# Optimization experiments

Hardware: AMD Instinct MI355X
Metric: run time of the kernel (lower is better)

## Reference

```python
import jax, jax.numpy as jnp
import numpy as np

B, D = 256, 1024
EPS = 1e-6


def setup_inputs() -> dict:
    key = jax.random.key(0)
    ks = jax.random.split(key, 8)
    s = 1.0 / np.sqrt(D)
    return {
        "x": jax.random.normal(ks[0], (B, D), jnp.float32),
        "Wq": jax.random.normal(ks[1], (D, D), jnp.float32) * s,
        "bq": jax.random.normal(ks[2], (D,), jnp.float32) * 0.01,
        "Wk": jax.random.normal(ks[3], (D, D), jnp.float32) * s,
        "bk": jax.random.normal(ks[4], (D,), jnp.float32) * 0.01,
        "Wv": jax.random.normal(ks[5], (D, D), jnp.float32) * s,
        "bv": jax.random.normal(ks[6], (D,), jnp.float32) * 0.01,
        "scale": jnp.asarray(1.0, jnp.float32),
        "norm_w": jnp.ones((D,), jnp.float32),
    }


def reference(x, Wq, bq, Wk, bk, Wv, bv, scale, norm_w):
    # QKV projections (torch Linear: x @ W.T + b)
    Q = x @ Wq.T + bq  # [B, D]
    K = x @ Wk.T + bk  # [B, D]
    V = x @ Wv.T + bv  # [B, D]
    # outer-product scores [B, D, D]: scores[b,i,j] = Q[b,i]*K[b,j]/scale
    scores = (Q[:, :, None] * K[:, None, :]) / scale
    attn = jax.nn.softmax(scores, axis=-1)  # [B, D, D]
    attended = jnp.einsum("bij,bj->bi", attn, V)  # [B, D]
    # dropout is identity in eval mode
    h = attended + x
    rms = jnp.sqrt(jnp.mean(h * h, axis=-1, keepdims=True) + EPS)
    return (h / rms) * norm_w
```

## Files before the change

### kernel.cpp

```cpp
#include <hip/hip_runtime.h>
#include <hip/hip_bf16.h>

#define BB 256
#define DD 1024

typedef unsigned short u16;
typedef unsigned int   u32;
typedef __attribute__((ext_vector_type(8))) __bf16 bf16x8;
typedef __attribute__((ext_vector_type(4))) float  floatx4;

__device__ __forceinline__ float bf2f(u16 u) {
    union { u32 i; float f; } t; t.i = ((u32)u) << 16; return t.f;
}
__device__ __forceinline__ u16 f2bf_rne(float f) {
    u32 u = __float_as_uint(f);
    u32 r = u + 0x7FFFu + ((u >> 16) & 1u);
    return (u16)(r >> 16);
}
__device__ __forceinline__ bool detect_bf16(const void* p) {
    return (*(const u32*)p) == 0x3F803F80u;
}
__device__ __forceinline__ float loadf(const void* p, int i, bool bf) {
    return bf ? bf2f(((const u16*)p)[i]) : ((const float*)p)[i];
}

__device__ __forceinline__ float wave_sum64(float x) {
    x += __int_as_float(__builtin_amdgcn_update_dpp(0, __float_as_int(x), 0x111, 0xF, 0xF, true));
    x += __int_as_float(__builtin_amdgcn_update_dpp(0, __float_as_int(x), 0x112, 0xF, 0xF, true));
    x += __int_as_float(__builtin_amdgcn_update_dpp(0, __float_as_int(x), 0x114, 0xF, 0xF, true));
    x += __int_as_float(__builtin_amdgcn_update_dpp(0, __float_as_int(x), 0x118, 0xF, 0xF, true));
    x += __int_as_float(__builtin_amdgcn_update_dpp(0, __float_as_int(x), 0x142, 0xA, 0xF, true));
    x += __int_as_float(__builtin_amdgcn_update_dpp(0, __float_as_int(x), 0x143, 0xC, 0xF, true));
    return x;
}

__device__ __forceinline__ void split1(float f, u16& h, u16& l) {
    u32 u  = __float_as_uint(f);
    u32 hu = u & 0xFFFF0000u;
    h = (u16)(hu >> 16);
    l = f2bf_rne(f - __uint_as_float(hu));
}

__global__ __launch_bounds__(256) void qkv_gemm(
    const void* __restrict__ x,
    const void* __restrict__ Wq, const void* __restrict__ bq,
    const void* __restrict__ Wk, const void* __restrict__ bk,
    const void* __restrict__ Wv, const void* __restrict__ bv,
    const void* __restrict__ nw,
    float* __restrict__ qkv)
{
    const bool bf = detect_bf16(nw);
    const int z = blockIdx.z;
    const void* W    = (z == 0) ? Wq : (z == 1) ? Wk : Wv;
    const void* bias = (z == 0) ? bq : (z == 1) ? bk : bv;
    float* outp = qkv + (size_t)z * BB * DD;

    const int m0 = blockIdx.x * 32;
    const int n0 = blockIdx.y * 64;
    const int tid  = threadIdx.x;
    const int lane = tid & 63;
    const int wave = tid >> 6;
    const int wr = wave & 1, wc = wave >> 1;
    const int l15 = lane & 15, quad = lane >> 4;

    __shared__ __align__(16) u16 Ah[32][72], Al[32][72];
    __shared__ __align__(16) u16 Bh[64][72], Bl[64][72];

    const int arow = tid >> 4;
    const int acol = (tid & 15) * 4;

    floatx4 acc[2] = {(floatx4){0.f,0.f,0.f,0.f}, (floatx4){0.f,0.f,0.f,0.f}};

    float4 ar[2], br[4];
    auto ld4 = [&](const void* p, int idx) -> float4 {
        if (!bf) return *(const float4*)((const float*)p + idx);
        const u16* q = (const u16*)p + idx;
        return make_float4(bf2f(q[0]), bf2f(q[1]), bf2f(q[2]), bf2f(q[3]));
    };
    auto fetch = [&](int k0) {
        #pragma unroll
        for (int f = 0; f < 2; ++f) ar[f] = ld4(x, (m0 + arow + f * 16) * DD + k0 + acol);
        #pragma unroll
        for (int f = 0; f < 4; ++f) br[f] = ld4(W, (n0 + arow + f * 16) * DD + k0 + acol);
    };

    fetch(0);
    for (int k0 = 0; k0 < DD; k0 += 64) {
        #pragma unroll
        for (int f = 0; f < 2; ++f) {
            const int r = arow + f * 16;
            ushort4 h, l;
            split1(ar[f].x, h.x, l.x); split1(ar[f].y, h.y, l.y);
            split1(ar[f].z, h.z, l.z); split1(ar[f].w, h.w, l.w);
            *(ushort4*)&Ah[r][acol] = h;
            *(ushort4*)&Al[r][acol] = l;
        }
        #pragma unroll
        for (int f = 0; f < 4; ++f) {
            const int r = arow + f * 16;
            ushort4 h, l;
            split1(br[f].x, h.x, l.x); split1(br[f].y, h.y, l.y);
            split1(br[f].z, h.z, l.z); split1(br[f].w, h.w, l.w);
            *(ushort4*)&Bh[r][acol] = h;
            *(ushort4*)&Bl[r][acol] = l;
        }
        __syncthreads();

        fetch((k0 + 64) & (DD - 1));

        #pragma unroll
        for (int kk = 0; kk < 2; ++kk) {
            const int ko = kk * 32 + quad * 8;
            const bf16x8 ah = *(const bf16x8*)&Ah[wr * 16 + l15][ko];
            const bf16x8 al = *(const bf16x8*)&Al[wr * 16 + l15][ko];
            #pragma unroll
            for (int ni = 0; ni < 2; ++ni) {
                const int brow = wc * 32 + ni * 16 + l15;
                const bf16x8 bh = *(const bf16x8*)&Bh[brow][ko];
                const bf16x8 bl = *(const bf16x8*)&Bl[brow][ko];
                acc[ni] = __builtin_amdgcn_mfma_f32_16x16x32_bf16(al, bh, acc[ni], 0, 0, 0);
                acc[ni] = __builtin_amdgcn_mfma_f32_16x16x32_bf16(ah, bl, acc[ni], 0, 0, 0);
                acc[ni] = __builtin_amdgcn_mfma_f32_16x16x32_bf16(ah, bh, acc[ni], 0, 0, 0);
            }
        }
        __syncthreads();
    }

    #pragma unroll
    for (int ni = 0; ni < 2; ++ni) {
        const int ng = n0 + wc * 32 + ni * 16 + l15;
        const float bv_ = loadf(bias, ng, bf);
        #pragma unroll
        for (int reg = 0; reg < 4; ++reg) {
            const int mg = m0 + wr * 16 + quad * 4 + reg;
            outp[mg * DD + ng] = acc[ni][reg] + bv_;
        }
    }
}

__global__ __launch_bounds__(1024) void attn_norm(
    const float* __restrict__ qkv,
    const void* __restrict__ x,
    const void* __restrict__ scale_p,
    const void* __restrict__ norm_w,
    void* __restrict__ out)
{
    const bool bf = detect_bf16(norm_w);
    const int b = blockIdx.x;
    const int tid = threadIdx.x;
    const int lane = tid & 63;
    const int wave = tid >> 6;

    __shared__ __align__(16) float2 kv[DD];
    __shared__ float wsum[16];

    const float* Qp = qkv + (size_t)b * DD;
    const float* Kp = Qp + (size_t)BB * DD;
    const float* Vp = Qp + 2 * (size_t)BB * DD;
    const float cvt = 1.44269504088896f / loadf(scale_p, 0, bf);

    kv[tid] = make_float2(Kp[tid] * cvt, Vp[tid]);
    __syncthreads();

    const float q   = Qp[tid];
    const float x_l = loadf(x, b * DD + tid, bf);

    float S0 = 0.f, S1 = 0.f, S2 = 0.f, S3 = 0.f;
    float T0 = 0.f, T1 = 0.f, T2 = 0.f, T3 = 0.f;
    const float4* kv4 = (const float4*)kv;
    for (int m = 0; m < DD / 2; m += 4) {
        const float4 p0 = kv4[m + 0];
        const float4 p1 = kv4[m + 1];
        const float4 p2 = kv4[m + 2];
        const float4 p3 = kv4[m + 3];
        float e;
        e = __builtin_amdgcn_exp2f(q * p0.x); S0 += e; T0 = fmaf(e, p0.y, T0);
        e = __builtin_amdgcn_exp2f(q * p0.z); S1 += e; T1 = fmaf(e, p0.w, T1);
        e = __builtin_amdgcn_exp2f(q * p1.x); S2 += e; T2 = fmaf(e, p1.y, T2);
        e = __builtin_amdgcn_exp2f(q * p1.z); S3 += e; T3 = fmaf(e, p1.w, T3);
        e = __builtin_amdgcn_exp2f(q * p2.x); S0 += e; T0 = fmaf(e, p2.y, T0);
        e = __builtin_amdgcn_exp2f(q * p2.z); S1 += e; T1 = fmaf(e, p2.w, T1);
        e = __builtin_amdgcn_exp2f(q * p3.x); S2 += e; T2 = fmaf(e, p3.y, T2);
        e = __builtin_amdgcn_exp2f(q * p3.z); S3 += e; T3 = fmaf(e, p3.w, T3);
    }
    const float S = (S0 + S1) + (S2 + S3);
    const float T = (T0 + T1) + (T2 + T3);
    const float h = fmaf(T, __builtin_amdgcn_rcpf(S), x_l);

    const float ss = wave_sum64(h * h);
    if (lane == 63) wsum[wave] = ss;
    __syncthreads();
    float tot = 0.f;
    #pragma unroll
    for (int w = 0; w < 16; ++w) tot += wsum[w];
    const float rinv = __builtin_amdgcn_rsqf(tot * (1.0f / DD) + 1e-6f);
    const float val = h * rinv * loadf(norm_w, tid, bf);
    const size_t oi = (size_t)b * DD + tid;
    if (bf) ((u16*)out)[oi] = f2bf_rne(val);
    else    ((float*)out)[oi] = val;
}

extern "C" void kernel_launch(void* const* d_in, const int* in_sizes, int n_in,
                              void* d_out, int out_size, void* d_ws, size_t ws_size,
                              hipStream_t stream) {
    const void* x  = d_in[0];
    const void* Wq = d_in[1];
    const void* bq = d_in[2];
    const void* Wk = d_in[3];
    const void* bk = d_in[4];
    const void* Wv = d_in[5];
    const void* bv = d_in[6];
    const void* sc = d_in[7];
    const void* nw = d_in[8];

    float* qkv = (float*)d_ws;

    qkv_gemm<<<dim3(8, 16, 3), 256, 0, stream>>>(x, Wq, bq, Wk, bk, Wv, bv, nw, qkv);
    attn_norm<<<dim3(BB), 1024, 0, stream>>>(qkv, x, sc, nw, d_out);
}
```

Before: 132.6 us.

## Pre-split inputs to bf16 hi/lo and run split-term GEMMs with atomic accumulation

Adds a prepass kernel that converts x and the three weight matrices into bf16 high/low halves in workspace and seeds the QKV output with biases. A new LDS-free GEMM reads the pre-split operands straight from global memory into registers with double-buffered fetches, and runs each of the three split products (lo*hi, hi*lo, hi*hi) as separate grid slices that atomically add into the output. The attention kernel drops its shared K/V staging and reads K/V directly from global memory with 8 accumulators. This trades redundant per-tile splitting and LDS traffic for an extra pass over the weights, more launches, and float atomics that make summation order nondeterministic.

```diff
diff --git a/kernel.cpp b/kernel.cpp
--- a/kernel.cpp
+++ b/kernel.cpp
@@ -22,6 +22,22 @@
 }
 __device__ __forceinline__ float loadf(const void* p, int i, bool bf) {
     return bf ? bf2f(((const u16*)p)[i]) : ((const float*)p)[i];
+}
+__device__ __forceinline__ float4 ld4(const void* p, int idx, bool bf) {
+    if (!bf) return *(const float4*)((const float*)p + idx);
+    const u16* q = (const u16*)p + idx;
+    return make_float4(bf2f(q[0]), bf2f(q[1]), bf2f(q[2]), bf2f(q[3]));
+}
+
+__device__ __forceinline__ void split1(float f, u16& h, u16& l) {
+    u32 u  = __float_as_uint(f);
+    u32 hu = u & 0xFFFF0000u;
+    h = (u16)(hu >> 16);
+    l = f2bf_rne(f - __uint_as_float(hu));
+}
+__device__ __forceinline__ void split4(float4 f, ushort4& h, ushort4& l) {
+    split1(f.x, h.x, l.x); split1(f.y, h.y, l.y);
+    split1(f.z, h.z, l.z); split1(f.w, h.w, l.w);
 }
 
 __device__ __forceinline__ float wave_sum64(float x) {
@@ -34,11 +50,108 @@
     return x;
 }
 
-__device__ __forceinline__ void split1(float f, u16& h, u16& l) {
-    u32 u  = __float_as_uint(f);
-    u32 hu = u & 0xFFFF0000u;
-    h = (u16)(hu >> 16);
-    l = f2bf_rne(f - __uint_as_float(hu));
+__global__ __launch_bounds__(256) void prepass(
+    const void* __restrict__ x,
+    const void* __restrict__ Wq, const void* __restrict__ Wk, const void* __restrict__ Wv,
+    const void* __restrict__ bq, const void* __restrict__ bk, const void* __restrict__ bv,
+    const void* __restrict__ nw,
+    float* __restrict__ qkv, u16* __restrict__ Xh, u16* __restrict__ Xl,
+    u16* __restrict__ Wh, u16* __restrict__ Wl)
+{
+    const bool bf = detect_bf16(nw);
+    const int idx = blockIdx.x * 256 + threadIdx.x;
+    if (idx < 65536) {
+        const int e = idx * 4;
+        ushort4 h, l; split4(ld4(x, e, bf), h, l);
+        *(ushort4*)(Xh + e) = h;
+        *(ushort4*)(Xl + e) = l;
+    } else if (idx < 65536 + 786432) {
+        const int i2 = idx - 65536;
+        const int wz = i2 >> 18;
+        const int e  = (i2 & 262143) * 4;
+        const void* W = (wz == 0) ? Wq : (wz == 1) ? Wk : Wv;
+        ushort4 h, l; split4(ld4(W, e, bf), h, l);
+        *(ushort4*)(Wh + wz * 1048576 + e) = h;
+        *(ushort4*)(Wl + wz * 1048576 + e) = l;
+    } else {
+        const int i3 = idx - (65536 + 786432);
+        const int z  = i3 >> 16;
+        const int e  = (i3 & 65535) * 4;
+        const void* B = (z == 0) ? bq : (z == 1) ? bk : bv;
+        *(float4*)(qkv + z * 262144 + e) = ld4(B, e & 1023, bf);
+    }
+}
+
+__global__ __launch_bounds__(256) void gemm_split(
+    const u16* __restrict__ Xh, const u16* __restrict__ Xl,
+    const u16* __restrict__ Wh, const u16* __restrict__ Wl,
+    float* __restrict__ qkv)
+{
+    const int seg = blockIdx.z / 3;
+    const int z   = blockIdx.z % 3;
+    const u16* Ap = (seg == 1) ? Xl : Xh;
+    const u16* Bp = ((seg == 2) ? Wl : Wh) + z * 1048576;
+    float* C = qkv + z * 262144;
+
+    const int m0 = blockIdx.x * 64, n0 = blockIdx.y * 64;
+    const int lane = threadIdx.x & 63;
+    const int wave = threadIdx.x >> 6;
+    const int wr = wave & 1, wc = wave >> 1;
+    const int l15 = lane & 15, quad = lane >> 4;
+
+    const u16* aRow[2]; const u16* bRow[2];
+    #pragma unroll
+    for (int mi = 0; mi < 2; ++mi) aRow[mi] = Ap + (m0 + wr * 32 + mi * 16 + l15) * DD + quad * 8;
+    #pragma unroll
+    for (int ni = 0; ni < 2; ++ni) bRow[ni] = Bp + (n0 + wc * 32 + ni * 16 + l15) * DD + quad * 8;
+
+    floatx4 acc[2][2];
+    #pragma unroll
+    for (int mi = 0; mi < 2; ++mi)
+        #pragma unroll
+        for (int ni = 0; ni < 2; ++ni)
+            acc[mi][ni] = (floatx4){0.f, 0.f, 0.f, 0.f};
+
+    bf16x8 fa0[2][2], fb0[2][2], fa1[2][2], fb1[2][2];
+    auto fetch = [&](bf16x8 (&fa)[2][2], bf16x8 (&fb)[2][2], int k0) {
+        #pragma unroll
+        for (int kk = 0; kk < 2; ++kk) {
+            #pragma unroll
+            for (int mi = 0; mi < 2; ++mi) fa[kk][mi] = *(const bf16x8*)(aRow[mi] + k0 + kk * 32);
+            #pragma unroll
+            for (int ni = 0; ni < 2; ++ni) fb[kk][ni] = *(const bf16x8*)(bRow[ni] + k0 + kk * 32);
+        }
+    };
+    auto compute = [&](bf16x8 (&fa)[2][2], bf16x8 (&fb)[2][2]) {
+        #pragma unroll
+        for (int kk = 0; kk < 2; ++kk)
+            #pragma unroll
+            for (int mi = 0; mi < 2; ++mi)
+                #pragma unroll
+                for (int ni = 0; ni < 2; ++ni)
+                    acc[mi][ni] = __builtin_amdgcn_mfma_f32_16x16x32_bf16(
+                        fa[kk][mi], fb[kk][ni], acc[mi][ni], 0, 0, 0);
+    };
+
+    fetch(fa0, fb0, 0);
+    for (int k0 = 0; k0 < DD; k0 += 128) {
+        fetch(fa1, fb1, k0 + 64);
+        compute(fa0, fb0);
+        if (k0 + 128 < DD) fetch(fa0, fb0, k0 + 128);
+        compute(fa1, fb1);
+    }
+
+    #pragma unroll
+    for (int ni = 0; ni < 2; ++ni) {
+        const int ng = n0 + wc * 32 + ni * 16 + l15;
+        #pragma unroll
+        for (int mi = 0; mi < 2; ++mi)
+            #pragma unroll
+            for (int reg = 0; reg < 4; ++reg) {
+                const int mg = m0 + wr * 32 + mi * 16 + quad * 4 + reg;
+                atomicAdd(&C[mg * DD + ng], acc[mi][ni][reg]);
+            }
+    }
 }
 
 __global__ __launch_bounds__(256) void qkv_gemm(
@@ -72,42 +185,29 @@
     floatx4 acc[2] = {(floatx4){0.f,0.f,0.f,0.f}, (floatx4){0.f,0.f,0.f,0.f}};
 
     float4 ar[2], br[4];
-    auto ld4 = [&](const void* p, int idx) -> float4 {
-        if (!bf) return *(const float4*)((const float*)p + idx);
-        const u16* q = (const u16*)p + idx;
-        return make_float4(bf2f(q[0]), bf2f(q[1]), bf2f(q[2]), bf2f(q[3]));
-    };
     auto fetch = [&](int k0) {
         #pragma unroll
-        for (int f = 0; f < 2; ++f) ar[f] = ld4(x, (m0 + arow + f * 16) * DD + k0 + acol);
-        #pragma unroll
-        for (int f = 0; f < 4; ++f) br[f] = ld4(W, (n0 + arow + f * 16) * DD + k0 + acol);
+        for (int f = 0; f < 2; ++f) ar[f] = ld4(x, (m0 + arow + f * 16) * DD + k0 + acol, bf);
+        #pragma unroll
+        for (int f = 0; f < 4; ++f) br[f] = ld4(W, (n0 + arow + f * 16) * DD + k0 + acol, bf);
     };
 
     fetch(0);
     for (int k0 = 0; k0 < DD; k0 += 64) {
         #pragma unroll
         for (int f = 0; f < 2; ++f) {
-            const int r = arow + f * 16;
-            ushort4 h, l;
-            split1(ar[f].x, h.x, l.x); split1(ar[f].y, h.y, l.y);
-            split1(ar[f].z, h.z, l.z); split1(ar[f].w, h.w, l.w);
-            *(ushort4*)&Ah[r][acol] = h;
-            *(ushort4*)&Al[r][acol] = l;
+            ushort4 h, l; split4(ar[f], h, l);
+            *(ushort4*)&Ah[arow + f * 16][acol] = h;
+            *(ushort4*)&Al[arow + f * 16][acol] = l;
         }
         #pragma unroll
         for (int f = 0; f < 4; ++f) {
-            const int r = arow + f * 16;
-            ushort4 h, l;
-            split1(br[f].x, h.x, l.x); split1(br[f].y, h.y, l.y);
-            split1(br[f].z, h.z, l.z); split1(br[f].w, h.w, l.w);
-            *(ushort4*)&Bh[r][acol] = h;
-            *(ushort4*)&Bl[r][acol] = l;
+            ushort4 h, l; split4(br[f], h, l);
+            *(ushort4*)&Bh[arow + f * 16][acol] = h;
+            *(ushort4*)&Bl[arow + f * 16][acol] = l;
         }
         __syncthreads();
-
         fetch((k0 + 64) & (DD - 1));
-
         #pragma unroll
         for (int kk = 0; kk < 2; ++kk) {
             const int ko = kk * 32 + quad * 8;
@@ -125,7 +225,6 @@
         }
         __syncthreads();
     }
-
     #pragma unroll
     for (int ni = 0; ni < 2; ++ni) {
         const int ng = n0 + wc * 32 + ni * 16 + l15;
@@ -151,42 +250,32 @@
     const int lane = tid & 63;
     const int wave = tid >> 6;
 
-    __shared__ __align__(16) float2 kv[DD];
-    __shared__ float wsum[16];
-
     const float* Qp = qkv + (size_t)b * DD;
     const float* Kp = Qp + (size_t)BB * DD;
     const float* Vp = Qp + 2 * (size_t)BB * DD;
+
     const float cvt = 1.44269504088896f / loadf(scale_p, 0, bf);
-
-    kv[tid] = make_float2(Kp[tid] * cvt, Vp[tid]);
-    __syncthreads();
-
-    const float q   = Qp[tid];
+    const float qc  = Qp[tid] * cvt;
     const float x_l = loadf(x, b * DD + tid, bf);
 
-    float S0 = 0.f, S1 = 0.f, S2 = 0.f, S3 = 0.f;
-    float T0 = 0.f, T1 = 0.f, T2 = 0.f, T3 = 0.f;
-    const float4* kv4 = (const float4*)kv;
-    for (int m = 0; m < DD / 2; m += 4) {
-        const float4 p0 = kv4[m + 0];
-        const float4 p1 = kv4[m + 1];
-        const float4 p2 = kv4[m + 2];
-        const float4 p3 = kv4[m + 3];
-        float e;
-        e = __builtin_amdgcn_exp2f(q * p0.x); S0 += e; T0 = fmaf(e, p0.y, T0);
-        e = __builtin_amdgcn_exp2f(q * p0.z); S1 += e; T1 = fmaf(e, p0.w, T1);
-        e = __builtin_amdgcn_exp2f(q * p1.x); S2 += e; T2 = fmaf(e, p1.y, T2);
-        e = __builtin_amdgcn_exp2f(q * p1.z); S3 += e; T3 = fmaf(e, p1.w, T3);
-        e = __builtin_amdgcn_exp2f(q * p2.x); S0 += e; T0 = fmaf(e, p2.y, T0);
-        e = __builtin_amdgcn_exp2f(q * p2.z); S1 += e; T1 = fmaf(e, p2.w, T1);
-        e = __builtin_amdgcn_exp2f(q * p3.x); S2 += e; T2 = fmaf(e, p3.y, T2);
-        e = __builtin_amdgcn_exp2f(q * p3.z); S3 += e; T3 = fmaf(e, p3.w, T3);
-    }
-    const float S = (S0 + S1) + (S2 + S3);
-    const float T = (T0 + T1) + (T2 + T3);
-    const float h = fmaf(T, __builtin_amdgcn_rcpf(S), x_l);
-
+    float S[8], T[8];
+    #pragma unroll
+    for (int u = 0; u < 8; ++u) { S[u] = 0.f; T[u] = 0.f; }
+
+    #pragma unroll 2
+    for (int j = 0; j < DD; j += 8) {
+        #pragma unroll
+        for (int u = 0; u < 8; ++u) {
+            const float e = __builtin_amdgcn_exp2f(qc * Kp[j + u]);
+            S[u] += e;
+            T[u] = fmaf(e, Vp[j + u], T[u]);
+        }
+    }
+    const float Ssum = ((S[0] + S[1]) + (S[2] + S[3])) + ((S[4] + S[5]) + (S[6] + S[7]));
+    const float Tsum = ((T[0] + T[1]) + (T[2] + T[3])) + ((T[4] + T[5]) + (T[6] + T[7]));
+    const float h = fmaf(Tsum, __builtin_amdgcn_rcpf(Ssum), x_l);
+
+    __shared__ float wsum[16];
     const float ss = wave_sum64(h * h);
     if (lane == 63) wsum[wave] = ss;
     __syncthreads();
@@ -215,6 +304,16 @@
 
     float* qkv = (float*)d_ws;
 
-    qkv_gemm<<<dim3(8, 16, 3), 256, 0, stream>>>(x, Wq, bq, Wk, bk, Wv, bv, nw, qkv);
+    if (ws_size >= (size_t)16 * 1024 * 1024) {
+        u16* Xh = (u16*)(qkv + 786432);
+        u16* Xl = Xh + 262144;
+        u16* Wh = Xl + 262144;
+        u16* Wl = Wh + 3 * 1048576;
+        prepass<<<dim3(4096), 256, 0, stream>>>(x, Wq, Wk, Wv, bq, bk, bv, nw,
+                                                qkv, Xh, Xl, Wh, Wl);
+        gemm_split<<<dim3(4, 16, 9), 256, 0, stream>>>(Xh, Xl, Wh, Wl, qkv);
+    } else {
+        qkv_gemm<<<dim3(8, 16, 3), 256, 0, stream>>>(x, Wq, bq, Wk, bk, Wv, bv, nw, qkv);
+    }
     attn_norm<<<dim3(BB), 1024, 0, stream>>>(qkv, x, sc, nw, d_out);
 }
```

Measured after the change: 161.0 us. 21.4% more time.

## Split attention into finer blocks, separate RMSNorm kernel, skip low split for bf16

Applied to the files above, without the earlier changes.

The 1024-thread-per-batch attention+norm kernel becomes a 256-thread kernel launched four times per batch row. Each block recomputes the K/V staging and writes the residual sum in place over Q, and a new finalize kernel does the RMS normalisation with vectorised loads and stores. The goal is better occupancy and more independent accumulators in the exp-heavy inner loop, paid for with an extra launch and a global round trip. The GEMM also drops the low-part bf16 split and its two extra MFMAs when inputs are bf16, but the default fp32 inputs do not take that path.

```diff
diff --git a/kernel.cpp b/kernel.cpp
--- a/kernel.cpp
+++ b/kernel.cpp
@@ -23,7 +23,21 @@
 __device__ __forceinline__ float loadf(const void* p, int i, bool bf) {
     return bf ? bf2f(((const u16*)p)[i]) : ((const float*)p)[i];
 }
-
+__device__ __forceinline__ float4 ld4(const void* p, int idx, bool bf) {
+    if (!bf) return *(const float4*)((const float*)p + idx);
+    const ushort4 q = *(const ushort4*)((const u16*)p + idx);
+    return make_float4(bf2f(q.x), bf2f(q.y), bf2f(q.z), bf2f(q.w));
+}
+__device__ __forceinline__ void split1(float f, u16& h, u16& l) {
+    u32 u  = __float_as_uint(f);
+    u32 hu = u & 0xFFFF0000u;
+    h = (u16)(hu >> 16);
+    l = f2bf_rne(f - __uint_as_float(hu));
+}
+__device__ __forceinline__ void split4(float4 f, ushort4& h, ushort4& l) {
+    split1(f.x, h.x, l.x); split1(f.y, h.y, l.y);
+    split1(f.z, h.z, l.z); split1(f.w, h.w, l.w);
+}
 __device__ __forceinline__ float wave_sum64(float x) {
     x += __int_as_float(__builtin_amdgcn_update_dpp(0, __float_as_int(x), 0x111, 0xF, 0xF, true));
     x += __int_as_float(__builtin_amdgcn_update_dpp(0, __float_as_int(x), 0x112, 0xF, 0xF, true));
@@ -32,13 +46,6 @@
     x += __int_as_float(__builtin_amdgcn_update_dpp(0, __float_as_int(x), 0x142, 0xA, 0xF, true));
     x += __int_as_float(__builtin_amdgcn_update_dpp(0, __float_as_int(x), 0x143, 0xC, 0xF, true));
     return x;
-}
-
-__device__ __forceinline__ void split1(float f, u16& h, u16& l) {
-    u32 u  = __float_as_uint(f);
-    u32 hu = u & 0xFFFF0000u;
-    h = (u16)(hu >> 16);
-    l = f2bf_rne(f - __uint_as_float(hu));
 }
 
 __global__ __launch_bounds__(256) void qkv_gemm(
@@ -57,9 +64,7 @@
 
     const int m0 = blockIdx.x * 32;
     const int n0 = blockIdx.y * 64;
-    const int tid  = threadIdx.x;
-    const int lane = tid & 63;
-    const int wave = tid >> 6;
+    const int tid = threadIdx.x, lane = tid & 63, wave = tid >> 6;
     const int wr = wave & 1, wc = wave >> 1;
     const int l15 = lane & 15, quad = lane >> 4;
 
@@ -72,54 +77,43 @@
     floatx4 acc[2] = {(floatx4){0.f,0.f,0.f,0.f}, (floatx4){0.f,0.f,0.f,0.f}};
 
     float4 ar[2], br[4];
-    auto ld4 = [&](const void* p, int idx) -> float4 {
-        if (!bf) return *(const float4*)((const float*)p + idx);
-        const u16* q = (const u16*)p + idx;
-        return make_float4(bf2f(q[0]), bf2f(q[1]), bf2f(q[2]), bf2f(q[3]));
-    };
     auto fetch = [&](int k0) {
         #pragma unroll
-        for (int f = 0; f < 2; ++f) ar[f] = ld4(x, (m0 + arow + f * 16) * DD + k0 + acol);
-        #pragma unroll
-        for (int f = 0; f < 4; ++f) br[f] = ld4(W, (n0 + arow + f * 16) * DD + k0 + acol);
+        for (int f = 0; f < 2; ++f) ar[f] = ld4(x, (m0 + arow + f * 16) * DD + k0 + acol, bf);
+        #pragma unroll
+        for (int f = 0; f < 4; ++f) br[f] = ld4(W, (n0 + arow + f * 16) * DD + k0 + acol, bf);
     };
 
     fetch(0);
     for (int k0 = 0; k0 < DD; k0 += 64) {
         #pragma unroll
         for (int f = 0; f < 2; ++f) {
-            const int r = arow + f * 16;
-            ushort4 h, l;
-            split1(ar[f].x, h.x, l.x); split1(ar[f].y, h.y, l.y);
-            split1(ar[f].z, h.z, l.z); split1(ar[f].w, h.w, l.w);
-            *(ushort4*)&Ah[r][acol] = h;
-            *(ushort4*)&Al[r][acol] = l;
+            ushort4 h, l; split4(ar[f], h, l);
+            *(ushort4*)&Ah[arow + f * 16][acol] = h;
+            if (!bf) *(ushort4*)&Al[arow + f * 16][acol] = l;
         }
         #pragma unroll
         for (int f = 0; f < 4; ++f) {
-            const int r = arow + f * 16;
-            ushort4 h, l;
-            split1(br[f].x, h.x, l.x); split1(br[f].y, h.y, l.y);
-            split1(br[f].z, h.z, l.z); split1(br[f].w, h.w, l.w);
-            *(ushort4*)&Bh[r][acol] = h;
-            *(ushort4*)&Bl[r][acol] = l;
+            ushort4 h, l; split4(br[f], h, l);
+            *(ushort4*)&Bh[arow + f * 16][acol] = h;
+            if (!bf) *(ushort4*)&Bl[arow + f * 16][acol] = l;
         }
         __syncthreads();
-
         fetch((k0 + 64) & (DD - 1));
-
         #pragma unroll
         for (int kk = 0; kk < 2; ++kk) {
             const int ko = kk * 32 + quad * 8;
             const bf16x8 ah = *(const bf16x8*)&Ah[wr * 16 + l15][ko];
-            const bf16x8 al = *(const bf16x8*)&Al[wr * 16 + l15][ko];
             #pragma unroll
             for (int ni = 0; ni < 2; ++ni) {
                 const int brow = wc * 32 + ni * 16 + l15;
                 const bf16x8 bh = *(const bf16x8*)&Bh[brow][ko];
-                const bf16x8 bl = *(const bf16x8*)&Bl[brow][ko];
-                acc[ni] = __builtin_amdgcn_mfma_f32_16x16x32_bf16(al, bh, acc[ni], 0, 0, 0);
-                acc[ni] = __builtin_amdgcn_mfma_f32_16x16x32_bf16(ah, bl, acc[ni], 0, 0, 0);
+                if (!bf) {
+                    const bf16x8 al = *(const bf16x8*)&Al[wr * 16 + l15][ko];
+                    const bf16x8 bl = *(const bf16x8*)&Bl[brow][ko];
+                    acc[ni] = __builtin_amdgcn_mfma_f32_16x16x32_bf16(al, bh, acc[ni], 0, 0, 0);
+                    acc[ni] = __builtin_amdgcn_mfma_f32_16x16x32_bf16(ah, bl, acc[ni], 0, 0, 0);
+                }
                 acc[ni] = __builtin_amdgcn_mfma_f32_16x16x32_bf16(ah, bh, acc[ni], 0, 0, 0);
             }
         }
@@ -138,66 +132,84 @@
     }
 }
 
-__global__ __launch_bounds__(1024) void attn_norm(
-    const float* __restrict__ qkv,
+__global__ __launch_bounds__(256) void attn_core(
+    float* __restrict__ qkv,
     const void* __restrict__ x,
     const void* __restrict__ scale_p,
+    const void* __restrict__ nw)
+{
+    const bool bf = detect_bf16(nw);
+    const int b   = blockIdx.x >> 2;
+    const int i   = (blockIdx.x & 3) * 256 + threadIdx.x;
+    const int tid = threadIdx.x;
+
+    float* Qp = qkv + (size_t)b * DD;
+    const float* Kp = Qp + (size_t)BB * DD;
+    const float* Vp = Qp + 2 * (size_t)BB * DD;
+
+    __shared__ __align__(16) float2 kv[DD];
+    const float cvt = 1.44269504088896f / loadf(scale_p, 0, bf);
+    #pragma unroll
+    for (int r = 0; r < 4; ++r) {
+        const int j = r * 256 + tid;
+        kv[j] = make_float2(Kp[j] * cvt, Vp[j]);
+    }
+    const float q   = Qp[i];
+    const float x_l = loadf(x, b * DD + i, bf);
+    __syncthreads();
+
+    float S[8], T[8];
+    #pragma unroll
+    for (int u = 0; u < 8; ++u) { S[u] = 0.f; T[u] = 0.f; }
+
+    const float4* kv4 = (const float4*)kv;
+    for (int m = 0; m < 512; m += 8) {
+        float4 p[8];
+        #pragma unroll
+        for (int t = 0; t < 8; ++t) p[t] = kv4[m + t];
+        #pragma unroll
+        for (int t = 0; t < 8; ++t) {
+            float e;
+            e = __builtin_amdgcn_exp2f(q * p[t].x); S[t] += e; T[t] = fmaf(e, p[t].y, T[t]);
+            e = __builtin_amdgcn_exp2f(q * p[t].z); S[t] += e; T[t] = fmaf(e, p[t].w, T[t]);
+        }
+    }
+    const float Ss = ((S[0]+S[1]) + (S[2]+S[3])) + ((S[4]+S[5]) + (S[6]+S[7]));
+    const float Ts = ((T[0]+T[1]) + (T[2]+T[3])) + ((T[4]+T[5]) + (T[6]+T[7]));
+    Qp[i] = fmaf(Ts, __builtin_amdgcn_rcpf(Ss), x_l);
+}
+
+__global__ __launch_bounds__(256) void finalize(
+    const float* __restrict__ qkv,
     const void* __restrict__ norm_w,
     void* __restrict__ out)
 {
     const bool bf = detect_bf16(norm_w);
     const int b = blockIdx.x;
     const int tid = threadIdx.x;
-    const int lane = tid & 63;
-    const int wave = tid >> 6;
-
-    __shared__ __align__(16) float2 kv[DD];
-    __shared__ float wsum[16];
-
-    const float* Qp = qkv + (size_t)b * DD;
-    const float* Kp = Qp + (size_t)BB * DD;
-    const float* Vp = Qp + 2 * (size_t)BB * DD;
-    const float cvt = 1.44269504088896f / loadf(scale_p, 0, bf);
-
-    kv[tid] = make_float2(Kp[tid] * cvt, Vp[tid]);
+    const int lane = tid & 63, wave = tid >> 6;
+    const float* hrow = qkv + (size_t)b * DD;
+
+    const float4 h4 = *(const float4*)(hrow + tid * 4);
+    const float ss = h4.x*h4.x + h4.y*h4.y + h4.z*h4.z + h4.w*h4.w;
+    __shared__ float wsum[4];
+    const float ws_ = wave_sum64(ss);
+    if (lane == 63) wsum[wave] = ws_;
     __syncthreads();
-
-    const float q   = Qp[tid];
-    const float x_l = loadf(x, b * DD + tid, bf);
-
-    float S0 = 0.f, S1 = 0.f, S2 = 0.f, S3 = 0.f;
-    float T0 = 0.f, T1 = 0.f, T2 = 0.f, T3 = 0.f;
-    const float4* kv4 = (const float4*)kv;
-    for (int m = 0; m < DD / 2; m += 4) {
-        const float4 p0 = kv4[m + 0];
-        const float4 p1 = kv4[m + 1];
-        const float4 p2 = kv4[m + 2];
-        const float4 p3 = kv4[m + 3];
-        float e;
-        e = __builtin_amdgcn_exp2f(q * p0.x); S0 += e; T0 = fmaf(e, p0.y, T0);
-        e = __builtin_amdgcn_exp2f(q * p0.z); S1 += e; T1 = fmaf(e, p0.w, T1);
-        e = __builtin_amdgcn_exp2f(q * p1.x); S2 += e; T2 = fmaf(e, p1.y, T2);
-        e = __builtin_amdgcn_exp2f(q * p1.z); S3 += e; T3 = fmaf(e, p1.w, T3);
-        e = __builtin_amdgcn_exp2f(q * p2.x); S0 += e; T0 = fmaf(e, p2.y, T0);
-        e = __builtin_amdgcn_exp2f(q * p2.z); S1 += e; T1 = fmaf(e, p2.w, T1);
-        e = __builtin_amdgcn_exp2f(q * p3.x); S2 += e; T2 = fmaf(e, p3.y, T2);
-        e = __builtin_amdgcn_exp2f(q * p3.z); S3 += e; T3 = fmaf(e, p3.w, T3);
-    }
-    const float S = (S0 + S1) + (S2 + S3);
-    const float T = (T0 + T1) + (T2 + T3);
-    const float h = fmaf(T, __builtin_amdgcn_rcpf(S), x_l);
-
-    const float ss = wave_sum64(h * h);
-    if (lane == 63) wsum[wave] = ss;
-    __syncthreads();
-    float tot = 0.f;
-    #pragma unroll
-    for (int w = 0; w < 16; ++w) tot += wsum[w];
+    const float tot = (wsum[0] + wsum[1]) + (wsum[2] + wsum[3]);
     const float rinv = __builtin_amdgcn_rsqf(tot * (1.0f / DD) + 1e-6f);
-    const float val = h * rinv * loadf(norm_w, tid, bf);
-    const size_t oi = (size_t)b * DD + tid;
-    if (bf) ((u16*)out)[oi] = f2bf_rne(val);
-    else    ((float*)out)[oi] = val;
+
+    float o[4];
+    #pragma unroll
+    for (int e = 0; e < 4; ++e)
+        o[e] = ((const float*)&h4)[e] * rinv * loadf(norm_w, tid * 4 + e, bf);
+    const size_t oi = (size_t)b * DD + tid * 4;
+    if (bf) {
+        ushort4 u = { f2bf_rne(o[0]), f2bf_rne(o[1]), f2bf_rne(o[2]), f2bf_rne(o[3]) };
+        *(ushort4*)((u16*)out + oi) = u;
+    } else {
+        *(float4*)((float*)out + oi) = make_float4(o[0], o[1], o[2], o[3]);
+    }
 }
 
 extern "C" void kernel_launch(void* const* d_in, const int* in_sizes, int n_in,
@@ -216,5 +228,6 @@
     float* qkv = (float*)d_ws;
 
     qkv_gemm<<<dim3(8, 16, 3), 256, 0, stream>>>(x, Wq, bq, Wk, bk, Wv, bv, nw, qkv);
-    attn_norm<<<dim3(BB), 1024, 0, stream>>>(qkv, x, sc, nw, d_out);
-}
+    attn_core<<<dim3(BB * 4), 256, 0, stream>>>(qkv, x, sc, nw);
+    finalize<<<dim3(BB), 256, 0, stream>>>(qkv, nw, d_out);
+}
```

Result: no change. 135.3 us (+2.0%).
